# Kernel tuning notes

Hardware: AMD Instinct MI355X
Metric: run time of the kernel (lower is better)

## Reference

```python
import jax, jax.numpy as jnp
import numpy as np

V, H, T, B, S = 50000, 256, 32, 64, 512


def setup_inputs() -> dict:
    key = jax.random.key(0)
    ks = jax.random.split(key, 16)
    sc = 0.05
    def n(k, shape):
        return jax.random.normal(k, shape, dtype=jnp.float32) * sc
    return {
        "seq": jax.random.randint(ks[0], (B, S), 0, V),
        "mask": jnp.ones((B, S), dtype=jnp.int32),
        "labels": jax.random.randint(ks[1], (B, S), 0, T),
        "embedding": n(ks[2], (V, H)),
        "Wih_f": n(ks[3], (4 * H, H)), "Whh_f": n(ks[4], (4 * H, H)),
        "bih_f": n(ks[5], (4 * H,)), "bhh_f": n(ks[6], (4 * H,)),
        "Wih_b": n(ks[7], (4 * H, H)), "Whh_b": n(ks[8], (4 * H, H)),
        "bih_b": n(ks[9], (4 * H,)), "bhh_b": n(ks[10], (4 * H,)),
        "fcW": n(ks[11], (T, 2 * H)), "fcb": n(ks[12], (T,)),
        "start_trans": n(ks[13], (T,)), "end_trans": n(ks[14], (T,)),
        "trans": n(ks[15], (T, T)),
    }


def _lstm_dir(x, Wih, Whh, bih, bhh, reverse):
    # x: [S,B,H]; torch LSTM gate order i,f,g,o
    Bz, Hh = x.shape[1], Whh.shape[1]
    def step(carry, xt):
        h, c = carry
        g = xt @ Wih.T + h @ Whh.T + bih + bhh  # [B,4H]
        i, f, gg, o = jnp.split(g, 4, axis=-1)
        c = jax.nn.sigmoid(f) * c + jax.nn.sigmoid(i) * jnp.tanh(gg)
        h = jax.nn.sigmoid(o) * jnp.tanh(c)
        return (h, c), h
    init = (jnp.zeros((Bz, Hh), x.dtype), jnp.zeros((Bz, Hh), x.dtype))
    _, hs = jax.lax.scan(step, init, x, reverse=reverse)
    return hs


def _crf_llh(em, tags, mask, start, end, trans):
    # em [S,B,T], tags [S,B] int, mask [S,B] bool -> scalar sum log-likelihood
    Sx, Bx, Tx = em.shape
    barange = jnp.arange(Bx)
    em_sc = jnp.take_along_axis(em, tags[:, :, None], axis=2)[..., 0]  # [S,B]
    m = mask.astype(em.dtype)
    num = start[tags[0]] + em_sc[0]
    tr_sc = trans[tags[:-1], tags[1:]]  # [S-1,B]
    num = num + jnp.sum((tr_sc + em_sc[1:]) * m[1:], axis=0)
    seq_ends = jnp.sum(mask.astype(jnp.int32), axis=0) - 1
    last_tags = tags[seq_ends, barange]
    num = num + end[last_tags]
    # forward algorithm (log-partition)
    def step(score, em_m):
        em_t, m_t = em_m
        nxt = jax.nn.logsumexp(score[:, :, None] + trans[None], axis=1) + em_t
        return jnp.where(m_t[:, None], nxt, score), None
    score0 = start[None] + em[0]
    score, _ = jax.lax.scan(step, score0, (em[1:], mask[1:]))
    den = jax.nn.logsumexp(score + end[None], axis=1)
    return jnp.sum(num - den)


def _viterbi(em, mask, start, end, trans):
    Sx, Bx, Tx = em.shape
    def step(score, em_m):
        em_t, m_t = em_m
        cand = score[:, :, None] + trans[None]  # [B,T_prev,T_cur]
        idx = jnp.argmax(cand, axis=1)
        nxt = jnp.max(cand, axis=1) + em_t
        idx = jnp.where(m_t[:, None], idx, jnp.arange(Tx)[None])
        return jnp.where(m_t[:, None], nxt, score), idx
    score0 = start[None] + em[0]
    score, hist = jax.lax.scan(step, score0, (em[1:], mask[1:]))  # hist [S-1,B,T]
    last = jnp.argmax(score + end[None], axis=1)  # [B]
    barange = jnp.arange(Bx)
    def back(tag, idx_t):
        prev = idx_t[barange, tag]
        return prev, prev
    _, prevs = jax.lax.scan(back, last, hist, reverse=True)  # prevs[k] = tag at time k
    return jnp.concatenate([prevs, last[None]], axis=0)  # [S,B]


def reference(seq, mask, labels, embedding, Wih_f, Whh_f, bih_f, bhh_f,
              Wih_b, Whh_b, bih_b, bhh_b, fcW, fcb,
              start_trans, end_trans, trans):
    x = seq.T  # [S,B] time-major as in original
    emb = embedding[x]  # [S,B,H]
    hf = _lstm_dir(emb, Wih_f, Whh_f, bih_f, bhh_f, False)
    hb = _lstm_dir(emb, Wih_b, Whh_b, bih_b, bhh_b, True)
    out = jnp.concatenate([hf, hb], axis=-1)  # [S,B,2H]
    logits = out @ fcW.T + fcb  # [S,B,T]; dropout is identity at eval
    m = mask.T.astype(bool)  # [S,B]
    loss = -_crf_llh(logits, labels.T, m, start_trans, end_trans, trans)
    preds = _viterbi(logits, m, start_trans, end_trans, trans)  # [S,B]
    return preds.T, loss
```

## Files before the change

### kernel.cpp

```cpp
#include <hip/hip_runtime.h>
#include <stdint.h>

#define SS 512
#define BB 64
#define HH 256
#define TT 32

typedef __attribute__((ext_vector_type(8))) short bf16x8;
typedef __attribute__((ext_vector_type(4))) short short4v;
typedef __attribute__((ext_vector_type(4))) float f32x4;

__device__ __forceinline__ unsigned short f2bf(float f){
  unsigned u = __float_as_uint(f);
  unsigned r = (u + 0x7FFFu + ((u >> 16) & 1u)) >> 16;
  return (unsigned short)r;
}
__device__ __forceinline__ float bf2f(unsigned short s){
  return __uint_as_float(((unsigned)s) << 16);
}
__device__ __forceinline__ float sigm(float x){ return 1.0f/(1.0f+__expf(-x)); }
__device__ __forceinline__ float ftanh(float x){
  float e = __expf(2.f*x);
  return 1.f - 2.f/(e + 1.f);
}
__device__ __forceinline__ unsigned cvt4fp8(float a0, float a1, float a2, float a3){
  int d = __builtin_amdgcn_cvt_pk_fp8_f32(a0, a1, 0, false);
  d = __builtin_amdgcn_cvt_pk_fp8_f32(a2, a3, d, true);
  return (unsigned)d;
}
__device__ __forceinline__ unsigned char cvt1fp8(float a){
  int d = __builtin_amdgcn_cvt_pk_fp8_f32(a, a, 0, false);
  return (unsigned char)(d & 0xFF);
}

__device__ __forceinline__ bf16x8 afrag(const unsigned short* A, int mt, int ktp, int nl, int kq){
  int m = mt*16 + nl;
  int sw = (m & 7) << 3;
  int kk = ktp*32 + kq*4;
  short4v lo = *(const short4v*)(A + (m << 8) + (kk ^ sw));
  short4v hi = *(const short4v*)(A + (m << 8) + ((kk + 16) ^ sw));
  bf16x8 r = {lo[0],lo[1],lo[2],lo[3],hi[0],hi[1],hi[2],hi[3]};
  return r;
}

__global__ __launch_bounds__(256,1) void k_xgemm(
    const int* __restrict__ seq, const float* __restrict__ emb,
    const float* __restrict__ Wih_f, const float* __restrict__ Wih_b,
    const float* __restrict__ bih_f, const float* __restrict__ bhh_f,
    const float* __restrict__ bih_b, const float* __restrict__ bhh_b,
    unsigned short* __restrict__ gx)
{
  __shared__ __align__(16) unsigned short A_l[128*256];
  __shared__ __align__(16) unsigned short B_l[64*256];

  const int tid = threadIdx.x;
  const int lane = tid & 63, w = tid >> 6;
  const int nl = lane & 15, kq = lane >> 4;
  const int pbase = blockIdx.x * 128;
  const int dir = blockIdx.y;
  const float* Wih  = dir ? Wih_b : Wih_f;
  const float* bihd = dir ? bih_b : bih_f;
  const float* bhhd = dir ? bhh_b : bhh_f;

#pragma unroll
  for (int i = 0; i < 16; ++i){
    int c = tid + i*256;
    int m = c >> 5, k8 = c & 31;
    int p = pbase + m, t = p >> 6, b = p & 63;
    int er = seq[b*SS + t];
    const float* s = emb + (size_t)er*HH + k8*8;
    float4 x0 = *(const float4*)s, x1 = *(const float4*)(s+4);
    union { unsigned short u[8]; uint4 v; } o;
    o.u[0]=f2bf(x0.x); o.u[1]=f2bf(x0.y); o.u[2]=f2bf(x0.z); o.u[3]=f2bf(x0.w);
    o.u[4]=f2bf(x1.x); o.u[5]=f2bf(x1.y); o.u[6]=f2bf(x1.z); o.u[7]=f2bf(x1.w);
    *(uint4*)&A_l[(m << 8) + ((k8*8) ^ ((m & 7) << 3))] = o.v;
  }

  for (int nb = 0; nb < 16; ++nb){
    __syncthreads();
#pragma unroll
    for (int i = 0; i < 8; ++i){
      int c = tid + i*256;
      int m = c >> 5, k8 = c & 31;
      const float* s = Wih + (size_t)(nb*64 + m)*HH + k8*8;
      float4 x0 = *(const float4*)s, x1 = *(const float4*)(s+4);
      union { unsigned short u[8]; uint4 v; } o;
      o.u[0]=f2bf(x0.x); o.u[1]=f2bf(x0.y); o.u[2]=f2bf(x0.z); o.u[3]=f2bf(x0.w);
      o.u[4]=f2bf(x1.x); o.u[5]=f2bf(x1.y); o.u[6]=f2bf(x1.z); o.u[7]=f2bf(x1.w);
      *(uint4*)&B_l[(m << 8) + ((k8*8) ^ ((m & 7) << 3))] = o.v;
    }
    __syncthreads();

    f32x4 acc[2][4];
#pragma unroll
    for (int mt = 0; mt < 2; ++mt)
#pragma unroll
      for (int nt = 0; nt < 4; ++nt) acc[mt][nt] = (f32x4){0.f,0.f,0.f,0.f};

#pragma unroll
    for (int kt = 0; kt < 8; ++kt){
      bf16x8 a0 = afrag(A_l, w*2+0, kt, nl, kq);
      bf16x8 a1 = afrag(A_l, w*2+1, kt, nl, kq);
#pragma unroll
      for (int nt = 0; nt < 4; ++nt){
        bf16x8 bv = afrag(B_l, nt, kt, nl, kq);
        acc[0][nt] = __builtin_amdgcn_mfma_f32_16x16x32_bf16(a0, bv, acc[0][nt], 0,0,0);
        acc[1][nt] = __builtin_amdgcn_mfma_f32_16x16x32_bf16(a1, bv, acc[1][nt], 0,0,0);
      }
    }

#pragma unroll
    for (int mt = 0; mt < 2; ++mt)
#pragma unroll
      for (int nt = 0; nt < 4; ++nt){
        int p0 = pbase + w*32 + mt*16 + kq*4;
        int t = p0 >> 6, b0 = p0 & 63;
        int col = nb*64 + nt*16 + nl;
        float bs = bihd[col] + bhhd[col];
        union { unsigned short u[4]; uint2 v; } o;
        o.u[0]=f2bf(acc[mt][nt][0] + bs); o.u[1]=f2bf(acc[mt][nt][1] + bs);
        o.u[2]=f2bf(acc[mt][nt][2] + bs); o.u[3]=f2bf(acc[mt][nt][3] + bs);
        *(uint2*)(gx + ((size_t)(dir*16 + (b0 >> 2))*SS + t)*4096 + col*4) = o.v;
      }
  }
}

#define WSC 64.0f
#define HSC 16.0f
#define ISC (1.0f/(WSC*HSC))

__global__ __launch_bounds__(1024,1) void k_lstm(
    const unsigned short* __restrict__ gx,
    const float* __restrict__ Whh_f, const float* __restrict__ Whh_b,
    unsigned short* __restrict__ hf, unsigned short* __restrict__ hb)
{
  __shared__ __align__(16) unsigned char h8[2][16][272];
  __shared__ __align__(16) float xch[16][4][16][4];

  const int tid  = threadIdx.x;
  const int lane = tid & 63;
  const int w    = tid >> 6;
  const int nl   = lane & 15;
  const int kq   = lane >> 4;
  const int dir  = blockIdx.x >> 4;
  const int bg   = blockIdx.x & 15;

  const float* Whh = dir ? Whh_b : Whh_f;
  unsigned short* hbuf = dir ? hb : hf;
  const unsigned short* gxd = gx + (size_t)(dir*16 + bg)*SS*4096;

  long wB[4][8];
#pragma unroll
  for (int g = 0; g < 4; ++g)
#pragma unroll
    for (int kt = 0; kt < 8; ++kt){
      int ncol = g*256 + w*16 + nl;
      const float* p = Whh + (size_t)ncol*HH + kt*32 + kq*4;
      float4 lo = *(const float4*)p;
      float4 hi = *(const float4*)(p + 16);
      union { unsigned d[2]; long l; } u;
      u.d[0] = cvt4fp8(lo.x*WSC, lo.y*WSC, lo.z*WSC, lo.w*WSC);
      u.d[1] = cvt4fp8(hi.x*WSC, hi.y*WSC, hi.z*WSC, hi.w*WSC);
      wB[g][kt] = u.l;
    }

  const int cc = w*16 + nl;
  const int hbyte = (cc >> 5)*32 + ((cc & 15) >> 2)*8 + ((cc & 16) ? 4 : 0) + (cc & 3);

  for (int i = tid; i < 2176; i += 1024) ((unsigned*)h8)[i] = 0;
  __syncthreads();

  float c0 = 0.f;

  unsigned short gxc[4], gxn[4];
  {
    const int t0 = dir ? (SS-1) : 0;
    const unsigned short* gp = gxd + (size_t)t0*4096;
#pragma unroll
    for (int g = 0; g < 4; ++g)
      gxc[g] = gp[(g*256 + cc)*4 + kq];
  }

  for (int s = 0; s < SS; ++s){
    const int t = dir ? (SS-1-s) : s;

    {
      int sn = s + 1;
      int tn = (sn < SS) ? (dir ? (SS-1-sn) : sn) : t;
      const unsigned short* gp = gxd + (size_t)tn*4096;
#pragma unroll
      for (int g = 0; g < 4; ++g)
        gxn[g] = gp[(g*256 + cc)*4 + kq];
    }

    const unsigned char* tp8 = &h8[s & 1][0][0];
    long af[8];
#pragma unroll
    for (int kt = 0; kt < 8; ++kt)
      af[kt] = *(const long*)(tp8 + nl*272 + kt*32 + kq*8);

    f32x4 acc[4];
#pragma unroll
    for (int g = 0; g < 4; ++g) acc[g] = (f32x4){0.f,0.f,0.f,0.f};

#pragma unroll
    for (int kt = 0; kt < 8; ++kt)
#pragma unroll
      for (int g = 0; g < 4; ++g)
        acc[g] = __builtin_amdgcn_mfma_f32_16x16x32_fp8_fp8(af[kt], wB[g][kt], acc[g], 0,0,0);

    if (kq == 0){
#pragma unroll
      for (int g = 0; g < 4; ++g)
        *(f32x4*)&xch[w][g][nl][0] = acc[g];
    }
    asm volatile("s_waitcnt lgkmcnt(0)" ::: "memory");

    {
      const int wslot = dir ? t : (s + 1);
      float i_ = xch[w][0][nl][kq]*ISC + bf2f(gxc[0]);
      float f_ = xch[w][1][nl][kq]*ISC + bf2f(gxc[1]);
      float g_ = xch[w][2][nl][kq]*ISC + bf2f(gxc[2]);
      float o_ = xch[w][3][nl][kq]*ISC + bf2f(gxc[3]);
      float cn = sigm(f_)*c0 + sigm(i_)*ftanh(g_);
      c0 = cn;
      float h = sigm(o_)*ftanh(cn);
      hbuf[(size_t)(wslot*BB + bg*4 + kq)*HH + cc] = f2bf(h);
      h8[(s + 1) & 1][kq][hbyte] = cvt1fp8(h*HSC);
    }

#pragma unroll
    for (int g = 0; g < 4; ++g) gxc[g] = gxn[g];

    asm volatile("s_waitcnt lgkmcnt(0)" ::: "memory");
    __builtin_amdgcn_s_barrier();
    asm volatile("" ::: "memory");
  }
}

__global__ __launch_bounds__(256,1) void k_fc(
    const unsigned short* __restrict__ hf, const unsigned short* __restrict__ hb,
    const float* __restrict__ fcW, const float* __restrict__ fcb,
    float* __restrict__ logits)
{
  __shared__ unsigned short Bs[32][516];
  __shared__ unsigned short Ah[4][32][260];
  __shared__ float fcb_s[32];
  const int tid = threadIdx.x;
  for (int i = tid; i < 32*512; i += 256){
    int tg = i >> 9, k = i & 511;
    Bs[tg][k] = f2bf(fcW[tg*512 + k]);
  }
  if (tid < 32) fcb_s[tid] = fcb[tid];
  __syncthreads();

  const int lane = tid & 63, w = tid >> 6;
  const int nl = lane & 15, kq = lane >> 4;
  const int pbase = blockIdx.x * 128;

  f32x4 acc[2][2];
#pragma unroll
  for (int mt = 0; mt < 2; ++mt)
#pragma unroll
    for (int nt = 0; nt < 2; ++nt) acc[mt][nt] = (f32x4){0.f,0.f,0.f,0.f};

  for (int half = 0; half < 2; ++half){
    for (int rr = 0; rr < 32; ++rr){
      int p = pbase + w*32 + rr;
      int t = p >> 6, b = p & 63;
      const unsigned short* src = half ? (hb + (size_t)(t*BB + b)*HH)
                                       : (hf + (size_t)((t+1)*BB + b)*HH);
      *(uint2*)&Ah[w][rr][lane*4] = *(const uint2*)(src + lane*4);
    }
#pragma unroll
    for (int kt = 0; kt < 8; ++kt){
      int kl = kt*32 + kq*4;
      bf16x8 a[2];
#pragma unroll
      for (int mt = 0; mt < 2; ++mt){
        const unsigned short* ar = &Ah[w][mt*16 + nl][kl];
        short4v lo = *(const short4v*)ar;
        short4v hi = *(const short4v*)(ar + 16);
        bf16x8 f = {lo[0],lo[1],lo[2],lo[3],hi[0],hi[1],hi[2],hi[3]};
        a[mt] = f;
      }
#pragma unroll
      for (int nt = 0; nt < 2; ++nt){
        const unsigned short* br = &Bs[nt*16 + nl][half*256 + kl];
        short4v lo = *(const short4v*)br;
        short4v hi = *(const short4v*)(br + 16);
        bf16x8 bv = {lo[0],lo[1],lo[2],lo[3],hi[0],hi[1],hi[2],hi[3]};
        acc[0][nt] = __builtin_amdgcn_mfma_f32_16x16x32_bf16(a[0], bv, acc[0][nt], 0,0,0);
        acc[1][nt] = __builtin_amdgcn_mfma_f32_16x16x32_bf16(a[1], bv, acc[1][nt], 0,0,0);
      }
    }
  }
#pragma unroll
  for (int mt = 0; mt < 2; ++mt)
#pragma unroll
    for (int nt = 0; nt < 2; ++nt)
#pragma unroll
      for (int r = 0; r < 4; ++r){
        int p = pbase + w*32 + mt*16 + kq*4 + r;
        int tg = nt*16 + nl;
        logits[(size_t)p*TT + tg] = acc[mt][nt][r] + fcb_s[tg];
      }
}

__global__ void k_crf(const float* __restrict__ logits, const int* __restrict__ mask,
                      const int* __restrict__ labels,
                      const float* __restrict__ start, const float* __restrict__ endt,
                      const float* __restrict__ trans,
                      float* __restrict__ den, float* __restrict__ num,
                      float* __restrict__ preds)
{
  __shared__ float tr[1024];
  __shared__ unsigned char vh_l[4][SS-1][32];
  const int tid = threadIdx.x;
  const int role = blockIdx.x >> 4;
  const int bq   = blockIdx.x & 15;
  if (role != 2){
    for (int i = tid; i < 1024; i += 256) tr[i] = trans[i];
    __syncthreads();
  }
  const int lane = tid & 63, w = tid >> 6;
  const int b = bq*4 + w;
  const int grp = lane >> 5, tp = lane & 31;

  if (role == 0){
    float score = start[tp] + logits[(size_t)b*TT + tp];
    float em_c = logits[(size_t)(BB + b)*TT + tp];
    int   mk_c = mask[b*SS + 1];
    for (int s = 1; s < SS; ++s){
      int sn = (s + 1 < SS) ? s + 1 : s;
      float em_n = logits[(size_t)(sn*BB + b)*TT + tp];
      int   mk_n = mask[b*SS + sn];
      float m = -1e30f;
#pragma unroll
      for (int jj = 0; jj < 16; ++jj){
        int j = grp*16 + jj;
        float v = __shfl(score, j) + tr[j*32 + tp];
        m = fmaxf(m, v);
      }
      m = fmaxf(m, __shfl_xor(m, 32));
      float ssum = 0.f;
#pragma unroll
      for (int jj = 0; jj < 16; ++jj){
        int j = grp*16 + jj;
        float v = __shfl(score, j) + tr[j*32 + tp];
        ssum += __expf(v - m);
      }
      ssum += __shfl_xor(ssum, 32);
      float ns = m + __logf(ssum) + em_c;
      score = mk_c ? ns : score;
      em_c = em_n; mk_c = mk_n;
    }
    float v = score + endt[tp];
    float mm = v;
    for (int d = 1; d < 32; d <<= 1) mm = fmaxf(mm, __shfl_xor(mm, d));
    float se = __expf(v - mm);
    for (int d = 1; d < 32; d <<= 1) se += __shfl_xor(se, d);
    if (lane == 0) den[b] = mm + __logf(se);
  } else if (role == 1){
    float score = start[tp] + logits[(size_t)b*TT + tp];
    float em_c = logits[(size_t)(BB + b)*TT + tp];
    int   mk_c = mask[b*SS + 1];
    for (int s = 1; s < SS; ++s){
      int sn = (s + 1 < SS) ? s + 1 : s;
      float em_n = logits[(size_t)(sn*BB + b)*TT + tp];
      int   mk_n = mask[b*SS + sn];
      float m = -1e30f; int am = 0;
#pragma unroll
      for (int jj = 0; jj < 16; ++jj){
        int j = grp*16 + jj;
        float v = __shfl(score, j) + tr[j*32 + tp];
        if (v > m){ m = v; am = j; }
      }
      float om = __shfl_xor(m, 32); int oam = __shfl_xor(am, 32);
      if (om > m || (om == m && oam < am)){ m = om; am = oam; }
      float ns = m + em_c;
      int idx = mk_c ? am : tp;
      if (grp == 0) vh_l[w][s-1][tp] = (unsigned char)idx;
      score = mk_c ? ns : score;
      em_c = em_n; mk_c = mk_n;
    }
    float v = score + endt[tp]; int a = tp;
    for (int d = 1; d < 32; d <<= 1){
      float ov = __shfl_xor(v, d); int oa = __shfl_xor(a, d);
      if (ov > v || (ov == v && oa < a)){ v = ov; a = oa; }
    }
    int tag = __shfl(a, 0);
    if (lane == 0) preds[(size_t)b*SS + SS - 1] = (float)tag;
    for (int s = SS - 1; s >= 1; --s){
      int rv = vh_l[w][s-1][tp];
      int pv = __shfl(rv, tag);
      if (lane == 0) preds[(size_t)b*SS + s - 1] = (float)pv;
      tag = pv;
    }
  } else {
    float acc = 0.f; int mcnt = 0;
    for (int s = lane; s < SS; s += 64){
      int mk = mask[b*SS + s];
      mcnt += mk;
      if (s >= 1){
        int tg = labels[b*SS + s], tpp = labels[b*SS + s - 1];
        float v = trans[tpp*32 + tg] + logits[(size_t)(s*BB + b)*TT + tg];
        acc += mk ? v : 0.f;
      }
    }
    for (int d = 1; d < 64; d <<= 1){ acc += __shfl_xor(acc, d); mcnt += __shfl_xor(mcnt, d); }
    if (lane == 0){
      int t0 = labels[b*SS];
      int tl = labels[b*SS + (mcnt - 1)];
      num[b] = start[t0] + logits[(size_t)b*TT + t0] + acc + endt[tl];
    }
  }
}

__global__ void k_loss(const float* __restrict__ num, const float* __restrict__ den,
                       float* __restrict__ out)
{
  int l = threadIdx.x;
  float v = num[l] - den[l];
  for (int d = 1; d < 64; d <<= 1) v += __shfl_xor(v, d);
  if (l == 0) out[BB*SS] = -v;
}

extern "C" void kernel_launch(void* const* d_in, const int* in_sizes, int n_in,
                              void* d_out, int out_size, void* d_ws, size_t ws_size,
                              hipStream_t stream)
{
  const int*   seq       = (const int*)  d_in[0];
  const int*   mask      = (const int*)  d_in[1];
  const int*   labels    = (const int*)  d_in[2];
  const float* embedding = (const float*)d_in[3];
  const float* Wih_f     = (const float*)d_in[4];
  const float* Whh_f     = (const float*)d_in[5];
  const float* bih_f     = (const float*)d_in[6];
  const float* bhh_f     = (const float*)d_in[7];
  const float* Wih_b     = (const float*)d_in[8];
  const float* Whh_b     = (const float*)d_in[9];
  const float* bih_b     = (const float*)d_in[10];
  const float* bhh_b     = (const float*)d_in[11];
  const float* fcW       = (const float*)d_in[12];
  const float* fcb       = (const float*)d_in[13];
  const float* start_t   = (const float*)d_in[14];
  const float* end_t     = (const float*)d_in[15];
  const float* trans     = (const float*)d_in[16];

  char* ws = (char*)d_ws;
  size_t off = 0;
  unsigned short* gxb = (unsigned short*)(ws + off); off += (size_t)2*SS*1024*64*2;
  unsigned short* hf  = (unsigned short*)(ws + off); off += (size_t)(SS+1)*BB*HH*2;
  unsigned short* hb  = (unsigned short*)(ws + off); off += (size_t)(SS+1)*BB*HH*2;
  float*          lgt = (float*)(ws + off);          off += (size_t)SS*BB*TT*4;
  float*          den = (float*)(ws + off);          off += 256;
  float*          num = (float*)(ws + off);          off += 256;

  k_xgemm<<<dim3(256,2), 256, 0, stream>>>(seq, embedding, Wih_f, Wih_b,
                                           bih_f, bhh_f, bih_b, bhh_b, gxb);
  k_lstm<<<32, 1024, 0, stream>>>(gxb, Whh_f, Whh_b, hf, hb);
  k_fc<<<256, 256, 0, stream>>>(hf, hb, fcW, fcb, lgt);
  k_crf<<<48, 256, 0, stream>>>(lgt, mask, labels, start_t, end_t, trans, den, num, (float*)d_out);
  k_loss<<<1, 64, 0, stream>>>(num, den, (float*)d_out);
}
```

Measured before the change: 1.449 ms.

## Use 16x16x128 scaled fp8 MFMA with packed h writeback in LSTM recurrence

Replaces eight 16x16x32 fp8 MFMAs per gate with two 16x16x128 scaled MFMAs (unit scales), re-laying out the fp8 recurrent weights and the h tile in LDS to match the wider K fragment. The fp8 h writes to LDS are packed via lane shuffles into 32-bit stores, and the bf16 h writes to global are paired into 32-bit stores. Index arithmetic is strength-reduced into pointer steps. This targets per-timestep latency on the serial recurrence, at the cost of extra shuffles and a new LDS layout that must match the MFMA operand format.

```diff
diff --git a/kernel.cpp b/kernel.cpp
--- a/kernel.cpp
+++ b/kernel.cpp
@@ -9,6 +9,8 @@
 typedef __attribute__((ext_vector_type(8))) short bf16x8;
 typedef __attribute__((ext_vector_type(4))) short short4v;
 typedef __attribute__((ext_vector_type(4))) float f32x4;
+typedef __attribute__((ext_vector_type(8))) int i32x8;
+typedef __attribute__((ext_vector_type(4))) int i32x4;
 
 __device__ __forceinline__ unsigned short f2bf(float f){
   unsigned u = __float_as_uint(f);
@@ -28,9 +30,9 @@
   d = __builtin_amdgcn_cvt_pk_fp8_f32(a2, a3, d, true);
   return (unsigned)d;
 }
-__device__ __forceinline__ unsigned char cvt1fp8(float a){
-  int d = __builtin_amdgcn_cvt_pk_fp8_f32(a, a, 0, false);
-  return (unsigned char)(d & 0xFF);
+__device__ __forceinline__ unsigned short cvt2fp8(float a0, float a1){
+  int d = __builtin_amdgcn_cvt_pk_fp8_f32(a0, a1, 0, false);
+  return (unsigned short)(d & 0xFFFF);
 }
 
 __device__ __forceinline__ bf16x8 afrag(const unsigned short* A, int mt, int ktp, int nl, int kq){
@@ -149,65 +151,68 @@
   unsigned short* hbuf = dir ? hb : hf;
   const unsigned short* gxd = gx + (size_t)(dir*16 + bg)*SS*4096;
 
-  long wB[4][8];
+  i32x8 wB[4][2];
 #pragma unroll
   for (int g = 0; g < 4; ++g)
 #pragma unroll
-    for (int kt = 0; kt < 8; ++kt){
+    for (int inst = 0; inst < 2; ++inst){
       int ncol = g*256 + w*16 + nl;
-      const float* p = Whh + (size_t)ncol*HH + kt*32 + kq*4;
-      float4 lo = *(const float4*)p;
-      float4 hi = *(const float4*)(p + 16);
-      union { unsigned d[2]; long l; } u;
-      u.d[0] = cvt4fp8(lo.x*WSC, lo.y*WSC, lo.z*WSC, lo.w*WSC);
-      u.d[1] = cvt4fp8(hi.x*WSC, hi.y*WSC, hi.z*WSC, hi.w*WSC);
-      wB[g][kt] = u.l;
+      i32x8 bfrag;
+#pragma unroll
+      for (int d = 0; d < 8; ++d){
+        int k0 = inst*128 + kq*32 + d*4;
+        float4 v = *(const float4*)(Whh + (size_t)ncol*HH + k0);
+        bfrag[d] = (int)cvt4fp8(v.x*WSC, v.y*WSC, v.z*WSC, v.w*WSC);
+      }
+      wB[g][inst] = bfrag;
     }
 
   const int cc = w*16 + nl;
-  const int hbyte = (cc >> 5)*32 + ((cc & 15) >> 2)*8 + ((cc & 16) ? 4 : 0) + (cc & 3);
 
   for (int i = tid; i < 2176; i += 1024) ((unsigned*)h8)[i] = 0;
   __syncthreads();
 
   float c0 = 0.f;
 
+  const int aoff = nl*272 + kq*32;
+  const int woff = kq*272 + w*16 + nl;
+  const ptrdiff_t gstep = dir ? -4096 : 4096;
+  const unsigned short* gbase = gxd + (size_t)(dir ? (SS-1) : 0)*4096 + cc*4 + kq;
+  unsigned short* hstore = hbuf + (size_t)(dir ? (SS-1) : 1)*BB*HH + (size_t)(bg*4 + kq)*HH + cc;
+  const ptrdiff_t hstep = (dir ? -(ptrdiff_t)1 : (ptrdiff_t)1)*BB*HH;
+
   unsigned short gxc[4], gxn[4];
-  {
-    const int t0 = dir ? (SS-1) : 0;
-    const unsigned short* gp = gxd + (size_t)t0*4096;
+#pragma unroll
+  for (int g = 0; g < 4; ++g) gxc[g] = gbase[g*1024];
+
+  for (int s = 0; s < SS; ++s){
+    const unsigned short* gnext = (s + 1 < SS) ? (gbase + gstep) : gbase;
+#pragma unroll
+    for (int g = 0; g < 4; ++g) gxn[g] = gnext[g*1024];
+
+    const unsigned char* tp8 = &h8[s & 1][0][0] + aoff;
+    i32x8 af0, af1;
+    {
+      i32x4 lo = *(const i32x4*)(tp8);
+      i32x4 hi = *(const i32x4*)(tp8 + 16);
+      af0 = (i32x8){lo[0],lo[1],lo[2],lo[3],hi[0],hi[1],hi[2],hi[3]};
+      i32x4 lo2 = *(const i32x4*)(tp8 + 128);
+      i32x4 hi2 = *(const i32x4*)(tp8 + 144);
+      af1 = (i32x8){lo2[0],lo2[1],lo2[2],lo2[3],hi2[0],hi2[1],hi2[2],hi2[3]};
+    }
+
+    f32x4 acc[4];
+#pragma unroll
+    for (int g = 0; g < 4; ++g) acc[g] = (f32x4){0.f,0.f,0.f,0.f};
+
 #pragma unroll
     for (int g = 0; g < 4; ++g)
-      gxc[g] = gp[(g*256 + cc)*4 + kq];
-  }
-
-  for (int s = 0; s < SS; ++s){
-    const int t = dir ? (SS-1-s) : s;
-
-    {
-      int sn = s + 1;
-      int tn = (sn < SS) ? (dir ? (SS-1-sn) : sn) : t;
-      const unsigned short* gp = gxd + (size_t)tn*4096;
-#pragma unroll
-      for (int g = 0; g < 4; ++g)
-        gxn[g] = gp[(g*256 + cc)*4 + kq];
-    }
-
-    const unsigned char* tp8 = &h8[s & 1][0][0];
-    long af[8];
-#pragma unroll
-    for (int kt = 0; kt < 8; ++kt)
-      af[kt] = *(const long*)(tp8 + nl*272 + kt*32 + kq*8);
-
-    f32x4 acc[4];
-#pragma unroll
-    for (int g = 0; g < 4; ++g) acc[g] = (f32x4){0.f,0.f,0.f,0.f};
-
-#pragma unroll
-    for (int kt = 0; kt < 8; ++kt)
-#pragma unroll
-      for (int g = 0; g < 4; ++g)
-        acc[g] = __builtin_amdgcn_mfma_f32_16x16x32_fp8_fp8(af[kt], wB[g][kt], acc[g], 0,0,0);
+      acc[g] = __builtin_amdgcn_mfma_scale_f32_16x16x128_f8f6f4(
+                 af0, wB[g][0], acc[g], 0, 0, 0, 0x7F7F7F7F, 0, 0x7F7F7F7F);
+#pragma unroll
+    for (int g = 0; g < 4; ++g)
+      acc[g] = __builtin_amdgcn_mfma_scale_f32_16x16x128_f8f6f4(
+                 af1, wB[g][1], acc[g], 0, 0, 0, 0x7F7F7F7F, 0, 0x7F7F7F7F);
 
     if (kq == 0){
 #pragma unroll
@@ -217,7 +222,6 @@
     asm volatile("s_waitcnt lgkmcnt(0)" ::: "memory");
 
     {
-      const int wslot = dir ? t : (s + 1);
       float i_ = xch[w][0][nl][kq]*ISC + bf2f(gxc[0]);
       float f_ = xch[w][1][nl][kq]*ISC + bf2f(gxc[1]);
       float g_ = xch[w][2][nl][kq]*ISC + bf2f(gxc[2]);
@@ -225,12 +229,25 @@
       float cn = sigm(f_)*c0 + sigm(i_)*ftanh(g_);
       c0 = cn;
       float h = sigm(o_)*ftanh(cn);
-      hbuf[(size_t)(wslot*BB + bg*4 + kq)*HH + cc] = f2bf(h);
-      h8[(s + 1) & 1][kq][hbyte] = cvt1fp8(h*HSC);
+
+      float s1 = __shfl_xor(h, 1);
+      unsigned short p01 = cvt2fp8(h*HSC, s1*HSC);
+      unsigned p23 = __shfl_xor((unsigned)p01, 2);
+      if ((nl & 3) == 0){
+        unsigned word = (unsigned)p01 | (p23 << 16);
+        *(unsigned*)(&h8[(s + 1) & 1][0][0] + woff) = word;
+      }
+      if (!(nl & 1)){
+        unsigned hv;
+        asm volatile("v_cvt_pk_bf16_f32 %0, %1, %2" : "=v"(hv) : "v"(h), "v"(s1));
+        *(unsigned*)hstore = hv;
+      }
     }
 
 #pragma unroll
     for (int g = 0; g < 4; ++g) gxc[g] = gxn[g];
+    gbase = gnext;
+    hstore += hstep;
 
     asm volatile("s_waitcnt lgkmcnt(0)" ::: "memory");
     __builtin_amdgcn_s_barrier();
```

New measurement: 1.385 ms. 4.4% less time.
